# Performance work log

Hardware: AMD Instinct MI355X
Metric: run time of the kernel (lower is better)

## Reference

```python
import jax, jax.numpy as jnp
import numpy as np

CHEBYSHEV_K = 5  # number of Chebyshev polynomial terms


def setup_inputs() -> dict:
    key = jax.random.key(0)
    k1, k2, k3 = jax.random.split(key, 3)
    B, N, F_in, F_out = 1024, 512, 16, 8
    x = jax.random.normal(k1, (B, N, F_in), dtype=jnp.float32)
    # symmetric scaled-Laplacian-like matrix, scaled small so recurrence stays stable
    A = jax.random.normal(k2, (N, N), dtype=jnp.float32) / jnp.sqrt(jnp.float32(N))
    L = 0.5 * (A + A.T)
    # xavier-uniform-like weights [K, F_in, F_out]
    limit = np.sqrt(6.0 / (F_in + F_out)).astype(np.float32)
    W = jax.random.uniform(k3, (CHEBYSHEV_K, F_in, F_out), dtype=jnp.float32,
                           minval=-limit, maxval=limit)
    b = jnp.zeros((F_out,), dtype=jnp.float32)
    return {"x": x, "L": L, "W": W, "b": b}


def reference(x, L, W, b):
    # x: [B, N, F_in], L: [N, N], W: [K, F_in, F_out], b: [F_out]
    Lx = lambda z: jnp.einsum('nm,bmf->bnf', L, z)
    Z0 = x
    Z1 = Lx(x)
    out = Z0 @ W[0] + Z1 @ W[1]
    for k in range(2, CHEBYSHEV_K):  # small fixed K, structural loop
        Zk = 2.0 * Lx(Z1) - Z0
        out = out + Zk @ W[k]
        Z0, Z1 = Z1, Zk
    return out + b
```

## Files before the change

### kernel.cpp

```cpp
#include <hip/hip_runtime.h>
#include <cstdint>
#include <cstddef>


typedef __attribute__((ext_vector_type(8))) short  frag_ab;
typedef __attribute__((ext_vector_type(4))) float  frag_cd;

constexpr int BN    = 512;
constexpr int FIN   = 16;
constexpr int FOUT  = 8;
constexpr int BT    = 4;
constexpr int NCOLS = BT * FIN;
constexpr int LDST  = BN + 8;
constexpr int ZBUF  = NCOLS * LDST;

__device__ __forceinline__ uint16_t f2bf(float f) {
    uint32_t u = __builtin_bit_cast(uint32_t, f);
    u += 0x7FFFu + ((u >> 16) & 1u);
    return (uint16_t)(u >> 16);
}
__device__ __forceinline__ float bf2f(uint16_t h) {
    uint32_t u = ((uint32_t)h) << 16;
    return __builtin_bit_cast(float, u);
}

__global__ void cvtL(const float* __restrict__ Lf, uint16_t* __restrict__ Lb) {
    int i = blockIdx.x * 256 + threadIdx.x;
    Lb[i] = f2bf(Lf[i]);
}

template <bool LBF16>
__global__ __launch_bounds__(512, 2)
void cheb_kernel(const float* __restrict__ x, const float* __restrict__ Lf,
                 const uint16_t* __restrict__ Lb, const float* __restrict__ W,
                 const float* __restrict__ bvec, float* __restrict__ out) {
    __shared__ uint16_t lds[2 * ZBUF];
    uint16_t* z0 = lds;
    uint16_t* z1 = lds + ZBUF;

    const int tid  = threadIdx.x;
    const int wave = tid >> 6;
    const int lane = tid & 63;
    const int lr   = lane & 15;
    const int q    = lane >> 4;

    const float4* x4 = reinterpret_cast<const float4*>(x + (size_t)blockIdx.x * (BT * BN * FIN));
    for (int s = 0; s < 2; ++s) {
        int a   = tid + s * 512;
        int f0g = a & 3;
        int n8  = (a >> 2) & 63;
        int bl  = a >> 8;
        int jb  = bl * 2048 + n8 * 32 + f0g;
        float4 v[8];
#pragma unroll
        for (int r = 0; r < 8; ++r) v[r] = x4[jb + r * 4];
        int cb = bl * 16 + f0g * 4;
        int nb = n8 * 8;
#pragma unroll
        for (int w = 0; w < 4; ++w) {
            frag_ab pk;
#pragma unroll
            for (int r = 0; r < 8; ++r)
                pk[r] = (short)f2bf(reinterpret_cast<const float*>(&v[r])[w]);
            *reinterpret_cast<frag_ab*>(&z0[(cb + w) * LDST + nb]) = pk;
        }
    }

    frag_ab wf[3];
#pragma unroll
    for (int p = 0; p < 3; ++p) {
        frag_ab t;
#pragma unroll
        for (int jj = 0; jj < 8; ++jj) {
            int k   = q * 8 + jj;
            int ki  = p * 2 + (k >> 4);
            int fin = k & 15;
            float val = (lr < 8 && ki < 5) ? W[ki * (FIN * FOUT) + fin * FOUT + lr] : 0.0f;
            t[jj] = (short)f2bf(val);
        }
        wf[p] = t;
    }
    const float bv = (lr < 8) ? bvec[lr] : 0.0f;

    frag_cd accOut[4][4] = {};

    auto loadA = [&](int mt, int ks) -> frag_ab {
        int row = mt * 16 + lr;
        int kb  = ks * 32 + q * 8;
        if constexpr (LBF16) {
            return *reinterpret_cast<const frag_ab*>(Lb + row * BN + kb);
        } else {
            const float4* p  = reinterpret_cast<const float4*>(Lf + row * BN + kb);
            float4 u0 = p[0], u1 = p[1];
            frag_ab t;
            t[0] = (short)f2bf(u0.x); t[1] = (short)f2bf(u0.y);
            t[2] = (short)f2bf(u0.z); t[3] = (short)f2bf(u0.w);
            t[4] = (short)f2bf(u1.x); t[5] = (short)f2bf(u1.y);
            t[6] = (short)f2bf(u1.z); t[7] = (short)f2bf(u1.w);
            return t;
        }
    };

    auto app = [&](const uint16_t* cur, uint16_t* dst, bool first) {
        frag_cd acc[4][4] = {};
        for (int ks = 0; ks < 16; ++ks) {
            frag_ab bfr[4];
#pragma unroll
            for (int ct = 0; ct < 4; ++ct)
                bfr[ct] = *reinterpret_cast<const frag_ab*>(
                    cur + (ct * 16 + lr) * LDST + ks * 32 + q * 8);
#pragma unroll
            for (int mi = 0; mi < 4; ++mi) {
                frag_ab a = loadA(wave + mi * 8, ks);
#pragma unroll
                for (int ct = 0; ct < 4; ++ct)
                    acc[mi][ct] = __builtin_amdgcn_mfma_f32_16x16x32_bf16(
                        a, bfr[ct], acc[mi][ct], 0, 0, 0);
            }
        }
#pragma unroll
        for (int mi = 0; mi < 4; ++mi) {
            int row0 = (wave + mi * 8) * 16 + q * 4;
#pragma unroll
            for (int ct = 0; ct < 4; ++ct) {
                uint16_t* dp = dst + (ct * 16 + lr) * LDST + row0;
                float pz[4] = {0.f, 0.f, 0.f, 0.f};
                if (!first) {
                    ushort4 pv = *reinterpret_cast<const ushort4*>(dp);
                    pz[0] = bf2f(pv.x); pz[1] = bf2f(pv.y);
                    pz[2] = bf2f(pv.z); pz[3] = bf2f(pv.w);
                }
                ushort4 nv;
                float v0 = acc[mi][ct][0], v1 = acc[mi][ct][1];
                float v2 = acc[mi][ct][2], v3 = acc[mi][ct][3];
                if (!first) {
                    v0 = 2.f * v0 - pz[0]; v1 = 2.f * v1 - pz[1];
                    v2 = 2.f * v2 - pz[2]; v3 = 2.f * v3 - pz[3];
                }
                nv.x = f2bf(v0); nv.y = f2bf(v1); nv.z = f2bf(v2); nv.w = f2bf(v3);
                *reinterpret_cast<ushort4*>(dp) = nv;
            }
        }
    };

    auto epi = [&](const uint16_t* bA, const uint16_t* bB, frag_ab wfr) {
        const uint16_t* base = (q < 2) ? bA : bB;
        int finb = (q & 1) * 8;
#pragma unroll
        for (int mi = 0; mi < 4; ++mi) {
            int n = (wave + mi * 8) * 16 + lr;
#pragma unroll
            for (int bt = 0; bt < 4; ++bt) {
                const uint16_t* pp = base + (bt * 16 + finb) * LDST + n;
                frag_ab afr;
#pragma unroll
                for (int jj = 0; jj < 8; ++jj) afr[jj] = (short)pp[jj * LDST];
                accOut[mi][bt] = __builtin_amdgcn_mfma_f32_16x16x32_bf16(
                    afr, wfr, accOut[mi][bt], 0, 0, 0);
            }
        }
    };

    __syncthreads();
    app(z0, z1, true);
    __syncthreads();
    epi(z0, z1, wf[0]);
    __syncthreads();
    app(z1, z0, false);
    __syncthreads();
    app(z0, z1, false);
    __syncthreads();
    epi(z0, z1, wf[1]);
    __syncthreads();
    app(z1, z0, false);
    __syncthreads();
    epi(z0, z0, wf[2]);

    if (lr < 8) {
        float* ob = out + (size_t)blockIdx.x * BT * BN * FOUT;
#pragma unroll
        for (int mi = 0; mi < 4; ++mi) {
            int row0 = (wave + mi * 8) * 16 + q * 4;
#pragma unroll
            for (int bt = 0; bt < 4; ++bt) {
                float* op = ob + bt * (BN * FOUT) + row0 * FOUT + lr;
                op[0 * FOUT] = accOut[mi][bt][0] + bv;
                op[1 * FOUT] = accOut[mi][bt][1] + bv;
                op[2 * FOUT] = accOut[mi][bt][2] + bv;
                op[3 * FOUT] = accOut[mi][bt][3] + bv;
            }
        }
    }
}

extern "C" void kernel_launch(void* const* d_in, const int* in_sizes, int n_in,
                              void* d_out, int out_size, void* d_ws, size_t ws_size,
                              hipStream_t stream) {
    const float* x  = (const float*)d_in[0];
    const float* Lf = (const float*)d_in[1];
    const float* W  = (const float*)d_in[2];
    const float* bv = (const float*)d_in[3];
    float* out = (float*)d_out;

    if (ws_size >= (size_t)(BN * BN * sizeof(uint16_t))) {
        uint16_t* Lb = (uint16_t*)d_ws;
        cvtL<<<dim3(1024), dim3(256), 0, stream>>>(Lf, Lb);
        cheb_kernel<true><<<dim3(256), dim3(512), 0, stream>>>(x, Lf, Lb, W, bv, out);
    } else {
        cheb_kernel<false><<<dim3(256), dim3(512), 0, stream>>>(x, Lf, nullptr, W, bv, out);
    }
}
```

Baseline: 156.4 us.

## Use 1024-thread blocks with software-pipelined A/B fragment loads

```diff
diff --git a/kernel.cpp b/kernel.cpp
--- a/kernel.cpp
+++ b/kernel.cpp
@@ -3,8 +3,9 @@
 #include <cstddef>
 
 
-typedef __attribute__((ext_vector_type(8))) short  frag_ab;
-typedef __attribute__((ext_vector_type(4))) float  frag_cd;
+typedef __attribute__((ext_vector_type(8))) short    frag_ab;
+typedef __attribute__((ext_vector_type(4))) float    frag_cd;
+typedef __attribute__((ext_vector_type(8))) uint16_t u16x8;
 
 constexpr int BN    = 512;
 constexpr int FIN   = 16;
@@ -13,6 +14,7 @@
 constexpr int NCOLS = BT * FIN;
 constexpr int LDST  = BN + 8;
 constexpr int ZBUF  = NCOLS * LDST;
+constexpr int ZOFF  = 16;
 
 __device__ __forceinline__ uint16_t f2bf(float f) {
     uint32_t u = __builtin_bit_cast(uint32_t, f);
@@ -26,17 +28,23 @@
 
 __global__ void cvtL(const float* __restrict__ Lf, uint16_t* __restrict__ Lb) {
     int i = blockIdx.x * 256 + threadIdx.x;
-    Lb[i] = f2bf(Lf[i]);
-}
-
-template <bool LBF16>
-__global__ __launch_bounds__(512, 2)
-void cheb_kernel(const float* __restrict__ x, const float* __restrict__ Lf,
-                 const uint16_t* __restrict__ Lb, const float* __restrict__ W,
-                 const float* __restrict__ bvec, float* __restrict__ out) {
-    __shared__ uint16_t lds[2 * ZBUF];
+    const float4* p = reinterpret_cast<const float4*>(Lf) + i * 2;
+    float4 u0 = p[0], u1 = p[1];
+    u16x8 o;
+    o[0] = f2bf(u0.x); o[1] = f2bf(u0.y);
+    o[2] = f2bf(u0.z); o[3] = f2bf(u0.w);
+    o[4] = f2bf(u1.x); o[5] = f2bf(u1.y);
+    o[6] = f2bf(u1.z); o[7] = f2bf(u1.w);
+    *(reinterpret_cast<u16x8*>(Lb) + i) = o;
+}
+
+__global__ __launch_bounds__(1024, 1)
+void cheb_kernel(const float* __restrict__ x, const uint16_t* __restrict__ Lb,
+                 const float* __restrict__ W, const float* __restrict__ bvec,
+                 float* __restrict__ out) {
+    __shared__ uint16_t lds[2 * ZBUF + ZOFF];
     uint16_t* z0 = lds;
-    uint16_t* z1 = lds + ZBUF;
+    uint16_t* z1 = lds + ZBUF + ZOFF;
 
     const int tid  = threadIdx.x;
     const int wave = tid >> 6;
@@ -45,8 +53,8 @@
     const int q    = lane >> 4;
 
     const float4* x4 = reinterpret_cast<const float4*>(x + (size_t)blockIdx.x * (BT * BN * FIN));
-    for (int s = 0; s < 2; ++s) {
-        int a   = tid + s * 512;
+    {
+        int a   = tid;
         int f0g = a & 3;
         int n8  = (a >> 2) & 63;
         int bl  = a >> 8;
@@ -82,61 +90,58 @@
     }
     const float bv = (lr < 8) ? bvec[lr] : 0.0f;
 
-    frag_cd accOut[4][4] = {};
-
-    auto loadA = [&](int mt, int ks) -> frag_ab {
-        int row = mt * 16 + lr;
-        int kb  = ks * 32 + q * 8;
-        if constexpr (LBF16) {
-            return *reinterpret_cast<const frag_ab*>(Lb + row * BN + kb);
-        } else {
-            const float4* p  = reinterpret_cast<const float4*>(Lf + row * BN + kb);
-            float4 u0 = p[0], u1 = p[1];
-            frag_ab t;
-            t[0] = (short)f2bf(u0.x); t[1] = (short)f2bf(u0.y);
-            t[2] = (short)f2bf(u0.z); t[3] = (short)f2bf(u0.w);
-            t[4] = (short)f2bf(u1.x); t[5] = (short)f2bf(u1.y);
-            t[6] = (short)f2bf(u1.z); t[7] = (short)f2bf(u1.w);
-            return t;
-        }
-    };
+    frag_cd accOut[2][4] = {};
+
+    const uint16_t* aBase0 = Lb + ((wave +  0) * 16 + lr) * BN + q * 8;
+    const uint16_t* aBase1 = Lb + ((wave + 16) * 16 + lr) * BN + q * 8;
 
     auto app = [&](const uint16_t* cur, uint16_t* dst, bool first) {
-        frag_cd acc[4][4] = {};
+        frag_cd acc[2][4] = {};
+        const uint16_t* bBase = cur + lr * LDST + q * 8;
+        frag_ab bf_[2][4];
+        frag_ab af_[3][2];
+
+        auto loadB = [&](int ks, int buf) {
+#pragma unroll
+            for (int ct = 0; ct < 4; ++ct)
+                bf_[buf][ct] = *reinterpret_cast<const frag_ab*>(
+                    bBase + ct * (16 * LDST) + ks * 32);
+        };
+        auto loadA = [&](int ks, int buf) {
+            af_[buf][0] = *reinterpret_cast<const frag_ab*>(aBase0 + ks * 32);
+            af_[buf][1] = *reinterpret_cast<const frag_ab*>(aBase1 + ks * 32);
+        };
+
+        loadB(0, 0);
+        loadA(0, 0);
+        loadA(1, 1);
+#pragma unroll
         for (int ks = 0; ks < 16; ++ks) {
-            frag_ab bfr[4];
-#pragma unroll
-            for (int ct = 0; ct < 4; ++ct)
-                bfr[ct] = *reinterpret_cast<const frag_ab*>(
-                    cur + (ct * 16 + lr) * LDST + ks * 32 + q * 8);
-#pragma unroll
-            for (int mi = 0; mi < 4; ++mi) {
-                frag_ab a = loadA(wave + mi * 8, ks);
+            const int cb = ks & 1, ab = ks % 3;
+            if (ks < 15) loadB(ks + 1, cb ^ 1);
+            if (ks < 14) loadA(ks + 2, (ks + 2) % 3);
+#pragma unroll
+            for (int mi = 0; mi < 2; ++mi)
 #pragma unroll
                 for (int ct = 0; ct < 4; ++ct)
                     acc[mi][ct] = __builtin_amdgcn_mfma_f32_16x16x32_bf16(
-                        a, bfr[ct], acc[mi][ct], 0, 0, 0);
-            }
-        }
-#pragma unroll
-        for (int mi = 0; mi < 4; ++mi) {
-            int row0 = (wave + mi * 8) * 16 + q * 4;
+                        af_[ab][mi], bf_[cb][ct], acc[mi][ct], 0, 0, 0);
+        }
+
+#pragma unroll
+        for (int mi = 0; mi < 2; ++mi) {
+            int row0 = (wave + mi * 16) * 16 + q * 4;
 #pragma unroll
             for (int ct = 0; ct < 4; ++ct) {
                 uint16_t* dp = dst + (ct * 16 + lr) * LDST + row0;
-                float pz[4] = {0.f, 0.f, 0.f, 0.f};
-                if (!first) {
-                    ushort4 pv = *reinterpret_cast<const ushort4*>(dp);
-                    pz[0] = bf2f(pv.x); pz[1] = bf2f(pv.y);
-                    pz[2] = bf2f(pv.z); pz[3] = bf2f(pv.w);
-                }
-                ushort4 nv;
                 float v0 = acc[mi][ct][0], v1 = acc[mi][ct][1];
                 float v2 = acc[mi][ct][2], v3 = acc[mi][ct][3];
                 if (!first) {
-                    v0 = 2.f * v0 - pz[0]; v1 = 2.f * v1 - pz[1];
-                    v2 = 2.f * v2 - pz[2]; v3 = 2.f * v3 - pz[3];
+                    ushort4 pv = *reinterpret_cast<const ushort4*>(dp);
+                    v0 = 2.f * v0 - bf2f(pv.x); v1 = 2.f * v1 - bf2f(pv.y);
+                    v2 = 2.f * v2 - bf2f(pv.z); v3 = 2.f * v3 - bf2f(pv.w);
                 }
+                ushort4 nv;
                 nv.x = f2bf(v0); nv.y = f2bf(v1); nv.z = f2bf(v2); nv.w = f2bf(v3);
                 *reinterpret_cast<ushort4*>(dp) = nv;
             }
@@ -147,8 +152,8 @@
         const uint16_t* base = (q < 2) ? bA : bB;
         int finb = (q & 1) * 8;
 #pragma unroll
-        for (int mi = 0; mi < 4; ++mi) {
-            int n = (wave + mi * 8) * 16 + lr;
+        for (int mi = 0; mi < 2; ++mi) {
+            int n = (wave + mi * 16) * 16 + lr;
 #pragma unroll
             for (int bt = 0; bt < 4; ++bt) {
                 const uint16_t* pp = base + (bt * 16 + finb) * LDST + n;
@@ -179,8 +184,8 @@
     if (lr < 8) {
         float* ob = out + (size_t)blockIdx.x * BT * BN * FOUT;
 #pragma unroll
-        for (int mi = 0; mi < 4; ++mi) {
-            int row0 = (wave + mi * 8) * 16 + q * 4;
+        for (int mi = 0; mi < 2; ++mi) {
+            int row0 = (wave + mi * 16) * 16 + q * 4;
 #pragma unroll
             for (int bt = 0; bt < 4; ++bt) {
                 float* op = ob + bt * (BN * FOUT) + row0 * FOUT + lr;
@@ -202,11 +207,7 @@
     const float* bv = (const float*)d_in[3];
     float* out = (float*)d_out;
 
-    if (ws_size >= (size_t)(BN * BN * sizeof(uint16_t))) {
-        uint16_t* Lb = (uint16_t*)d_ws;
-        cvtL<<<dim3(1024), dim3(256), 0, stream>>>(Lf, Lb);
-        cheb_kernel<true><<<dim3(256), dim3(512), 0, stream>>>(x, Lf, Lb, W, bv, out);
-    } else {
-        cheb_kernel<false><<<dim3(256), dim3(512), 0, stream>>>(x, Lf, nullptr, W, bv, out);
-    }
-}
+    uint16_t* Lb = (uint16_t*)d_ws;
+    cvtL<<<dim3(128), dim3(256), 0, stream>>>(Lf, Lb);
+    cheb_kernel<<<dim3(256), dim3(1024), 0, stream>>>(x, Lb, W, bv, out);
+}
```

After: 160.9 us. 1.03x slower.
